# Optimization experiments

Hardware: AMD Instinct MI355X
Metric: run time of the kernel (lower is better)

The kernel has to match this reference:

```python
import math
import jax, jax.numpy as jnp
import numpy as np

NH, NKV, HD, THETA = 32, 8, 128, 500000.0

def rotate_half(x):
    x1, x2 = jnp.split(x, 2, axis=-1)
    return jnp.concatenate((-x2, x1), axis=-1)

def rope_cos_sin(seq_len, dim, base, dtype):
    inv_freq = 1.0 / (base ** (jnp.arange(0, dim, 2, dtype=jnp.float32) / dim))
    t = jnp.arange(seq_len, dtype=jnp.float32)
    freqs = jnp.outer(t, inv_freq)              # [S, dim/2]
    emb = jnp.concatenate((freqs, freqs), -1)   # [S, dim]
    return jnp.cos(emb).astype(dtype), jnp.sin(emb).astype(dtype)

def setup_inputs() -> dict:
    key = jax.random.key(0)
    ks = jax.random.split(key, 5)
    B, S, H = 1, 2048, 4096
    sc = 1.0 / math.sqrt(H)
    return {
        'x':  jax.random.normal(ks[0], (B, S, H), jnp.float32),
        'wq': jax.random.normal(ks[1], (H, H), jnp.float32) * sc,
        'wk': jax.random.normal(ks[2], (NKV * HD, H), jnp.float32) * sc,
        'wv': jax.random.normal(ks[3], (NKV * HD, H), jnp.float32) * sc,
        'wo': jax.random.normal(ks[4], (H, H), jnp.float32) * sc,
    }

def attention(x, wq, wk, wv, wo):
    B, S, H = x.shape
    n_rep = NH // NKV
    q = (x @ wq.T).reshape(B, S, NH, HD).transpose(0, 2, 1, 3)    # [B,NH,S,HD]
    k = (x @ wk.T).reshape(B, S, NKV, HD).transpose(0, 2, 1, 3)   # [B,NKV,S,HD]
    v = (x @ wv.T).reshape(B, S, NKV, HD).transpose(0, 2, 1, 3)
    cos, sin = rope_cos_sin(S, HD, THETA, x.dtype)                # [S,HD]
    cos = cos[None, None]; sin = sin[None, None]
    q = q * cos + rotate_half(q) * sin
    k = k * cos + rotate_half(k) * sin
    k = jnp.repeat(k, n_rep, axis=1)                               # [B,NH,S,HD]
    v = jnp.repeat(v, n_rep, axis=1)
    scores = jnp.einsum('bhqd,bhkd->bhqk', q, k) / math.sqrt(HD)
    causal = jnp.tril(jnp.ones((S, S), dtype=bool))
    scores = jnp.where(causal, scores, jnp.finfo(scores.dtype).min)
    probs = jax.nn.softmax(scores, axis=-1)
    out = jnp.einsum('bhqk,bhkd->bhqd', probs, v)                  # [B,NH,S,HD]
    out = out.transpose(0, 2, 1, 3).reshape(B, S, H)
    return out @ wo.T

def reference(x, wq, wk, wv, wo):
    return attention(x, wq, wk, wv, wo)
```

## Files before the change

kernel.cpp:

```cpp
#include <hip/hip_runtime.h>
#include <hip/hip_bf16.h>
#include <math.h>

typedef __bf16 bf16x8 __attribute__((ext_vector_type(8)));
typedef __bf16 bf16x4 __attribute__((ext_vector_type(4)));
typedef unsigned short u16x8 __attribute__((ext_vector_type(8)));
typedef float  f32x4  __attribute__((ext_vector_type(4)));

constexpr int kS   = 2048;
constexpr int kH   = 4096;
constexpr int kNH  = 32;
constexpr int kNKV = 8;
constexpr int kHD  = 128;
constexpr int kQKV = kH + 2 * kNKV * kHD;
constexpr int kKOff = kH;
constexpr int kVOff = kH + kNKV * kHD;

__global__ void cast_bf16(const float* __restrict__ in, __bf16* __restrict__ out, int n4) {
    int i = blockIdx.x * blockDim.x + threadIdx.x;
    if (i < n4) {
        float4 f = ((const float4*)in)[i];
        bf16x4 o;
        o[0] = (__bf16)f.x; o[1] = (__bf16)f.y; o[2] = (__bf16)f.z; o[3] = (__bf16)f.w;
        ((bf16x4*)out)[i] = o;
    }
}

__global__ void cast_all(const float* __restrict__ x, const float* __restrict__ wq,
                         const float* __restrict__ wk, const float* __restrict__ wv,
                         __bf16* __restrict__ xb, __bf16* __restrict__ wqkv) {
    int i = blockIdx.x * 256 + threadIdx.x;
    float4 f;
    __bf16* dst;
    int di;
    if (i < (1 << 21)) {
        f = ((const float4*)x)[i];
        dst = xb; di = i;
    } else {
        int j = i - (1 << 21);
        const float4* s = (j < (1 << 22)) ? ((const float4*)wq + j)
                        : (j < (5 << 20)) ? ((const float4*)wk + (j - (1 << 22)))
                                          : ((const float4*)wv + (j - (5 << 20)));
        f = *s;
        dst = wqkv; di = j;
    }
    bf16x4 o;
    o[0] = (__bf16)f.x; o[1] = (__bf16)f.y; o[2] = (__bf16)f.z; o[3] = (__bf16)f.w;
    ((bf16x4*)dst)[di] = o;
}

__device__ inline void gld16(const __bf16* g, __bf16* l) {
    __builtin_amdgcn_global_load_lds((const __attribute__((address_space(1))) void*)g,
                                     (__attribute__((address_space(3))) void*)l, 16, 0, 0);
}

constexpr int GBK = 32, GBM = 128;

template <typename OutT, int GBN>
__global__ __launch_bounds__(512, 2) void gemm8(const __bf16* __restrict__ A,
                                                const __bf16* __restrict__ B,
                                                OutT* __restrict__ C,
                                                int M, int N, int K, int nbx) {
    constexpr int FM  = 4;
    constexpr int FN  = GBN / 64;
    constexpr int AL  = GBM / 128;
    constexpr int BL  = GBN / 128;
    constexpr int GPK = AL + BL;
    constexpr int ASZ = GBM * GBK;
    constexpr int BSZ = GBN * GBK;

    __shared__ __align__(16) __bf16 Ab[4][ASZ];
    __shared__ __align__(16) __bf16 Bb[4][BSZ];

    const int tid = threadIdx.x, w = tid >> 6, lane = tid & 63;
    const int lr = lane & 15, g = lane >> 4;

    const int nwg = (int)gridDim.x;
    const int bid = (int)blockIdx.x;
    const int id2 = (bid & 7) * (nwg >> 3) + (bid >> 3);
    const int m0 = (id2 / nbx) * GBM, n0 = (id2 % nbx) * GBN;

    const int wm = (w >> 2) * 64, wn = (w & 3) * (GBN / 4);

    const __bf16* ga[AL]; int la[AL];
    const __bf16* gb[BL]; int lb[BL];
#pragma unroll
    for (int a = 0; a < AL; a++) {
        int G = a * 512 + tid, row = G >> 2;
        int lg = (G & 3) ^ ((row >> 1) & 3);
        ga[a] = A + (size_t)(m0 + row) * K + lg * 8;
        la[a] = G * 8;
    }
#pragma unroll
    for (int b = 0; b < BL; b++) {
        int G = b * 512 + tid, row = G >> 2;
        int lg = (G & 3) ^ ((row >> 1) & 3);
        gb[b] = B + (size_t)(n0 + row) * K + lg * 8;
        lb[b] = G * 8;
    }

    int pao[FM], pbo[FN];
    const int sw = (lr >> 1) & 3;
#pragma unroll
    for (int i = 0; i < FM; i++) pao[i] = (wm + i * 16 + lr) * GBK + ((g ^ sw) * 8);
#pragma unroll
    for (int j = 0; j < FN; j++) pbo[j] = (wn + j * 16 + lr) * GBK + ((g ^ sw) * 8);

    f32x4 acc[FM][FN];
#pragma unroll
    for (int i = 0; i < FM; i++)
#pragma unroll
        for (int j = 0; j < FN; j++) acc[i][j] = (f32x4)(0.f);

    const int NT = K / GBK;

#pragma unroll
    for (int z = 0; z < 3; z++) {
#pragma unroll
        for (int a = 0; a < AL; a++) gld16(ga[a] + z * GBK, &Ab[z][la[a]]);
#pragma unroll
        for (int b = 0; b < BL; b++) gld16(gb[b] + z * GBK, &Bb[z][lb[b]]);
    }
    if constexpr (GPK == 4) asm volatile("s_waitcnt vmcnt(8)" ::: "memory");
    else                    asm volatile("s_waitcnt vmcnt(6)" ::: "memory");
    __builtin_amdgcn_s_barrier();

    for (int Z = 0; Z < NT; ++Z) {
        const int q = Z & 3, qs = (Z + 3) & 3;

        bf16x8 af[FM], bfr[FN];
#pragma unroll
        for (int i = 0; i < FM; i++) af[i]  = *(const bf16x8*)&Ab[q][pao[i]];
#pragma unroll
        for (int j = 0; j < FN; j++) bfr[j] = *(const bf16x8*)&Bb[q][pbo[j]];

        if (Z < NT - 3) {
#pragma unroll
            for (int a = 0; a < AL; a++) gld16(ga[a] + (Z + 3) * GBK, &Ab[qs][la[a]]);
#pragma unroll
            for (int b = 0; b < BL; b++) gld16(gb[b] + (Z + 3) * GBK, &Bb[qs][lb[b]]);
        }

        __builtin_amdgcn_s_barrier();
        __builtin_amdgcn_s_setprio(1);
#pragma unroll
        for (int i = 0; i < FM; i++)
#pragma unroll
            for (int j = 0; j < FN; j++)
                acc[i][j] = __builtin_amdgcn_mfma_f32_16x16x32_bf16(
                    af[i], bfr[j], acc[i][j], 0, 0, 0);
        __builtin_amdgcn_s_setprio(0);

        if (Z < NT - 3) {
            if constexpr (GPK == 4) asm volatile("s_waitcnt vmcnt(8)" ::: "memory");
            else                    asm volatile("s_waitcnt vmcnt(6)" ::: "memory");
        } else if (Z == NT - 3) {
            if constexpr (GPK == 4) asm volatile("s_waitcnt vmcnt(4)" ::: "memory");
            else                    asm volatile("s_waitcnt vmcnt(3)" ::: "memory");
        } else if (Z == NT - 2) {
            asm volatile("s_waitcnt vmcnt(0)" ::: "memory");
        }
        __builtin_amdgcn_s_barrier();
    }

    const int cr = g * 4, cc = lr;
#pragma unroll
    for (int i = 0; i < FM; i++)
#pragma unroll
        for (int j = 0; j < FN; j++) {
            OutT* Cp = C + (size_t)(m0 + wm + i * 16 + cr) * N + (n0 + wn + j * 16 + cc);
#pragma unroll
            for (int r = 0; r < 4; r++) Cp[(size_t)r * N] = (OutT)acc[i][j][r];
        }
}

__global__ void rope_qkv(__bf16* __restrict__ qkv) {
    int idx  = blockIdx.x * 256 + threadIdx.x;
    int d8   = idx & 7;
    int rest = idx >> 3;
    int hh   = rest % (kNH + kNKV);
    int s    = rest / (kNH + kNKV);
    __bf16* base = qkv + (size_t)s * kQKV + ((hh < kNH) ? hh * kHD : kKOff + (hh - kNH) * kHD);
    float sc = (hh < kNH) ? 0.088388347648318447f : 1.0f;
    bf16x8 va = *(const bf16x8*)(base + d8 * 8);
    bf16x8 vb = *(const bf16x8*)(base + 64 + d8 * 8);
    bf16x8 ra, rb;
#pragma unroll
    for (int j = 0; j < 8; j++) {
        int d = d8 * 8 + j;
        float rev = (float)s * exp2f(fmaf((float)d, -0.2958057589f, -2.6514961295f));
        rev -= floorf(rev);
        float ang = rev * 6.28318530718f;
        float sn = __sinf(ang), cs = __cosf(ang);
        float a = (float)va[j], b = (float)vb[j];
        ra[j] = (__bf16)((a * cs - b * sn) * sc);
        rb[j] = (__bf16)((b * cs + a * sn) * sc);
    }
    *(bf16x8*)(base + d8 * 8)      = ra;
    *(bf16x8*)(base + 64 + d8 * 8) = rb;
}

constexpr int VTP = 72;

__global__ __launch_bounds__(256) void flash_attn(const __bf16* __restrict__ qkv,
                                                  __bf16* __restrict__ ob) {
    __shared__ __align__(16) __bf16 Ks[64 * 128];
    __shared__ __align__(16) __bf16 Vt[128 * VTP];
    __shared__ __align__(16) __bf16 Ps[4 * 16 * 64];

    const int tid  = threadIdx.x;
    const int wave = tid >> 6, lane = tid & 63;
    const int bx   = blockIdx.x;
    const int kvh  = bx & 7;
    const int qt   = 127 - (bx >> 3);
    const int h    = kvh * 4 + wave;
    const int r    = lane & 15, g = lane >> 4;
    const int r7   = r & 7;
    const int qglob = qt * 16 + r;

    __bf16* Pw = Ps + wave * 16 * 64;
    const __bf16* kbase = qkv + kKOff + kvh * kHD;
    const __bf16* vbase = qkv + kVOff + kvh * kHD;

    int krow[4], kgc[4];
#pragma unroll
    for (int c = 0; c < 4; c++) {
        krow[c] = wave * 16 + c * 4 + (lane >> 4);
        kgc[c]  = (lane & 15) ^ (krow[c] & 15);
    }

    bf16x8 qfrag[4];
    const __bf16* qrow = qkv + (size_t)(qt * 16 + r) * kQKV + h * kHD + g * 8;
#pragma unroll
    for (int c = 0; c < 4; c++) qfrag[c] = *(const bf16x8*)(qrow + c * 32);

    f32x4 o[8];
#pragma unroll
    for (int dt = 0; dt < 8; dt++) o[dt] = (f32x4)(0.f);
    float mrow = -3.0e38f, lrow = 0.f;

    const int nkt = qt / 4 + 1;
    for (int kt = 0; kt < nkt; ++kt) {
#pragma unroll
        for (int c = 0; c < 4; c++)
            gld16(kbase + (size_t)(kt * 64 + krow[c]) * kQKV + kgc[c] * 8,
                  Ks + (wave * 4 + c) * 512);
#pragma unroll
        for (int i = 0; i < 2; i++) {
            int task = i * 256 + tid;
            int p = task & 31, c = task >> 5;
            const __bf16* v0 = vbase + (size_t)(kt * 64 + 2 * p) * kQKV + c * 8;
            u16x8 a = __builtin_bit_cast(u16x8, *(const bf16x8*)v0);
            u16x8 b = __builtin_bit_cast(u16x8, *(const bf16x8*)(v0 + kQKV));
#pragma unroll
            for (int j = 0; j < 8; j++) {
                unsigned int pk = (unsigned int)a[j] | ((unsigned int)b[j] << 16);
                *(unsigned int*)(Vt + (c * 8 + j) * VTP + 2 * p) = pk;
            }
        }
        __syncthreads();

        f32x4 st[4];
#pragma unroll
        for (int t = 0; t < 4; t++) st[t] = (f32x4)(0.f);
#pragma unroll
        for (int c = 0; c < 4; c++) {
#pragma unroll
            for (int t = 0; t < 4; t++) {
                bf16x8 kf = *(const bf16x8*)&Ks[(t * 16 + r) * 128 + (((c * 4 + g) ^ r) * 8)];
                st[t] = __builtin_amdgcn_mfma_f32_16x16x32_bf16(kf, qfrag[c], st[t], 0, 0, 0);
            }
        }

        if (kt == nkt - 1) {
#pragma unroll
            for (int t = 0; t < 4; t++)
#pragma unroll
                for (int reg = 0; reg < 4; reg++) {
                    int key = kt * 64 + t * 16 + g * 4 + reg;
                    if (key > qglob) st[t][reg] = -3.0e38f;
                }
        }

        float mloc = -3.0e38f;
#pragma unroll
        for (int t = 0; t < 4; t++)
#pragma unroll
            for (int reg = 0; reg < 4; reg++) mloc = fmaxf(mloc, st[t][reg]);
        mloc = fmaxf(mloc, __shfl_xor(mloc, 16));
        mloc = fmaxf(mloc, __shfl_xor(mloc, 32));
        float mnew  = fmaxf(mrow, mloc);
        float alpha = __expf(mrow - mnew);
        mrow = mnew;
        float lsum = 0.f;
#pragma unroll
        for (int t = 0; t < 4; t++)
#pragma unroll
            for (int reg = 0; reg < 4; reg++) {
                float pv = __expf(st[t][reg] - mnew);
                st[t][reg] = pv;
                lsum += pv;
            }
        lsum += __shfl_xor(lsum, 16);
        lsum += __shfl_xor(lsum, 32);
        lrow = lrow * alpha + lsum;

        float ar[4];
#pragma unroll
        for (int reg = 0; reg < 4; reg++) ar[reg] = __shfl(alpha, g * 4 + reg);
#pragma unroll
        for (int dt = 0; dt < 8; dt++)
#pragma unroll
            for (int reg = 0; reg < 4; reg++) o[dt][reg] *= ar[reg];

#pragma unroll
        for (int t = 0; t < 4; t++) {
            bf16x4 pb;
#pragma unroll
            for (int j = 0; j < 4; j++) pb[j] = (__bf16)st[t][j];
            int p8 = t * 4 + g;
            *(bf16x4*)&Pw[r * 64 + (((p8 >> 1) ^ r7) * 8) + ((p8 & 1) * 4)] = pb;
        }
        __asm__ volatile("s_waitcnt lgkmcnt(0)" ::: "memory");

#pragma unroll
        for (int kc = 0; kc < 2; kc++) {
            bf16x8 pf = *(const bf16x8*)&Pw[r * 64 + (((kc * 4 + g) ^ r7) * 8)];
#pragma unroll
            for (int dt = 0; dt < 8; dt++) {
                bf16x8 vf = *(const bf16x8*)&Vt[(dt * 16 + r) * VTP + kc * 32 + g * 8];
                o[dt] = __builtin_amdgcn_mfma_f32_16x16x32_bf16(pf, vf, o[dt], 0, 0, 0);
            }
        }
        __syncthreads();
    }

    float linv = 1.f / lrow;
    float lr4[4];
#pragma unroll
    for (int reg = 0; reg < 4; reg++) lr4[reg] = __shfl(linv, g * 4 + reg);
#pragma unroll
    for (int dt = 0; dt < 8; dt++)
#pragma unroll
        for (int reg = 0; reg < 4; reg++) {
            int qq = g * 4 + reg, dd = dt * 16 + r;
            ob[(size_t)(qt * 16 + qq) * kH + h * kHD + dd] = (__bf16)(o[dt][reg] * lr4[reg]);
        }
}

extern "C" void kernel_launch(void* const* d_in, const int* in_sizes, int n_in,
                              void* d_out, int out_size, void* d_ws, size_t ws_size,
                              hipStream_t stream) {
    const float* x  = (const float*)d_in[0];
    const float* wq = (const float*)d_in[1];
    const float* wk = (const float*)d_in[2];
    const float* wv = (const float*)d_in[3];
    const float* wo = (const float*)d_in[4];
    float* out = (float*)d_out;

    char* p = (char*)d_ws;
    auto alloc = [&](size_t bytes) {
        char* r = p;
        p += (bytes + 255) & ~(size_t)255;
        return r;
    };
    __bf16* xb    = (__bf16*)alloc((size_t)kS * kH * 2);
    __bf16* wqkvb = (__bf16*)alloc((size_t)kQKV * kH * 2);
    __bf16* qkv   = (__bf16*)alloc((size_t)kS * kQKV * 2);
    __bf16* ao    = xb;
    __bf16* wob   = wqkvb;

    cast_all<<<dim3(1 << 15), 256, 0, stream>>>(x, wq, wk, wv, xb, wqkvb);

    gemm8<__bf16, 384><<<dim3((kS / GBM) * (kQKV / 384)), 512, 0, stream>>>(
        xb, wqkvb, qkv, kS, kQKV, kH, kQKV / 384);

    rope_qkv<<<dim3(kS * (kNH + kNKV) * 8 / 256), 256, 0, stream>>>(qkv);

    cast_bf16<<<dim3((kH * kH / 4) / 256), 256, 0, stream>>>(wo, wob, kH * kH / 4);

    flash_attn<<<dim3(kNKV * (kS / 16)), 256, 0, stream>>>(qkv, ao);

    gemm8<float, 256><<<dim3((kS / GBM) * (kH / 256)), 512, 0, stream>>>(
        ao, wob, out, kS, kH, kH, kH / 256);
}
```

Before: 474.9 us.

## Split GEMM k-step into two half phases and remap tiles per XCD

Each k-iteration of the bf16 GEMM is split into two halves: first load A fragments and half the B fragments, issue A prefetches, run half the MFMAs, then load the rest of B and issue B prefetches before the second half of the MFMAs. This interleaves LDS reads and global-to-LDS loads with matrix math more finely, in the style of ping-pong scheduling. It also adds a special tile mapping for the 256-block, 16-column-tile case so that each XCD covers a compact 4x8 block of output tiles, which is meant to improve L2 reuse. The cost is an extra barrier per iteration.

```diff
diff --git a/kernel.cpp b/kernel.cpp
--- a/kernel.cpp
+++ b/kernel.cpp
@@ -63,6 +63,7 @@
                                                 int M, int N, int K, int nbx) {
     constexpr int FM  = 4;
     constexpr int FN  = GBN / 64;
+    constexpr int SH  = FN / 2;
     constexpr int AL  = GBM / 128;
     constexpr int BL  = GBN / 128;
     constexpr int GPK = AL + BL;
@@ -77,8 +78,16 @@
 
     const int nwg = (int)gridDim.x;
     const int bid = (int)blockIdx.x;
-    const int id2 = (bid & 7) * (nwg >> 3) + (bid >> 3);
-    const int m0 = (id2 / nbx) * GBM, n0 = (id2 % nbx) * GBN;
+    int trow, tcol;
+    if (nwg == 256 && nbx == 16) {
+        const int xcd = bid & 7, j = bid >> 3;
+        trow = (xcd >> 1) * 4 + (j >> 3);
+        tcol = (xcd & 1) * 8 + (j & 7);
+    } else {
+        const int id2 = (bid & 7) * (nwg >> 3) + (bid >> 3);
+        trow = id2 / nbx; tcol = id2 % nbx;
+    }
+    const int m0 = trow * GBM, n0 = tcol * GBN;
 
     const int wm = (w >> 2) * 64, wn = (w & 3) * (GBN / 4);
 
@@ -127,26 +136,40 @@
 
     for (int Z = 0; Z < NT; ++Z) {
         const int q = Z & 3, qs = (Z + 3) & 3;
+        const bool stg = Z < NT - 3;
 
         bf16x8 af[FM], bfr[FN];
 #pragma unroll
-        for (int i = 0; i < FM; i++) af[i]  = *(const bf16x8*)&Ab[q][pao[i]];
-#pragma unroll
-        for (int j = 0; j < FN; j++) bfr[j] = *(const bf16x8*)&Bb[q][pbo[j]];
-
-        if (Z < NT - 3) {
+        for (int i = 0; i < FM; i++) af[i] = *(const bf16x8*)&Ab[q][pao[i]];
+#pragma unroll
+        for (int j = 0; j < SH; j++) bfr[j] = *(const bf16x8*)&Bb[q][pbo[j]];
+        if (stg) {
 #pragma unroll
             for (int a = 0; a < AL; a++) gld16(ga[a] + (Z + 3) * GBK, &Ab[qs][la[a]]);
-#pragma unroll
-            for (int b = 0; b < BL; b++) gld16(gb[b] + (Z + 3) * GBK, &Bb[qs][lb[b]]);
-        }
-
+        }
         __builtin_amdgcn_s_barrier();
         __builtin_amdgcn_s_setprio(1);
 #pragma unroll
         for (int i = 0; i < FM; i++)
 #pragma unroll
-            for (int j = 0; j < FN; j++)
+            for (int j = 0; j < SH; j++)
+                acc[i][j] = __builtin_amdgcn_mfma_f32_16x16x32_bf16(
+                    af[i], bfr[j], acc[i][j], 0, 0, 0);
+        __builtin_amdgcn_s_setprio(0);
+        __builtin_amdgcn_s_barrier();
+
+#pragma unroll
+        for (int j = SH; j < FN; j++) bfr[j] = *(const bf16x8*)&Bb[q][pbo[j]];
+        if (stg) {
+#pragma unroll
+            for (int b = 0; b < BL; b++) gld16(gb[b] + (Z + 3) * GBK, &Bb[qs][lb[b]]);
+        }
+        __builtin_amdgcn_s_barrier();
+        __builtin_amdgcn_s_setprio(1);
+#pragma unroll
+        for (int i = 0; i < FM; i++)
+#pragma unroll
+            for (int j = SH; j < FN; j++)
                 acc[i][j] = __builtin_amdgcn_mfma_f32_16x16x32_bf16(
                     af[i], bfr[j], acc[i][j], 0, 0, 0);
         __builtin_amdgcn_s_setprio(0);
```

After: 488.7 us. +2.9%, slower.

## Double-buffer K/V tiles in flash attention and remap GEMM tiles per XCD

Applied to the files above, without the earlier changes.

The flash-attention kernel now keeps two shared-memory buffers for K and transposed V. It issues global loads for the next key tile before the current tile's QK and softmax work, then writes the transposed V into the alternate buffer, so memory latency overlaps compute. Separately, the GEMM tile mapping for the 256-workgroup, 16-column case assigns each XCD a compact 4x8 block of tiles to improve L2 locality. The cost is double the K/V shared memory, which may lower occupancy, plus extra registers held for the prefetched V.

```diff
diff --git a/kernel.cpp b/kernel.cpp
--- a/kernel.cpp
+++ b/kernel.cpp
@@ -77,8 +77,16 @@
 
     const int nwg = (int)gridDim.x;
     const int bid = (int)blockIdx.x;
-    const int id2 = (bid & 7) * (nwg >> 3) + (bid >> 3);
-    const int m0 = (id2 / nbx) * GBM, n0 = (id2 % nbx) * GBN;
+    int trow, tcol;
+    if (nwg == 256 && nbx == 16) {
+        const int xcd = bid & 7, j = bid >> 3;
+        trow = (xcd >> 1) * 4 + (j >> 3);
+        tcol = (xcd & 1) * 8 + (j & 7);
+    } else {
+        const int id2 = (bid & 7) * (nwg >> 3) + (bid >> 3);
+        trow = id2 / nbx; tcol = id2 % nbx;
+    }
+    const int m0 = trow * GBM, n0 = tcol * GBN;
 
     const int wm = (w >> 2) * 64, wn = (w & 3) * (GBN / 4);
 
@@ -204,8 +212,8 @@
 
 __global__ __launch_bounds__(256) void flash_attn(const __bf16* __restrict__ qkv,
                                                   __bf16* __restrict__ ob) {
-    __shared__ __align__(16) __bf16 Ks[64 * 128];
-    __shared__ __align__(16) __bf16 Vt[128 * VTP];
+    __shared__ __align__(16) __bf16 Ks[2][64 * 128];
+    __shared__ __align__(16) __bf16 Vt[2][128 * VTP];
     __shared__ __align__(16) __bf16 Ps[4 * 16 * 64];
 
     const int tid  = threadIdx.x;
@@ -228,6 +236,12 @@
         krow[c] = wave * 16 + c * 4 + (lane >> 4);
         kgc[c]  = (lane & 15) ^ (krow[c] & 15);
     }
+    int vp[2], vc[2];
+#pragma unroll
+    for (int i = 0; i < 2; i++) {
+        int task = i * 256 + tid;
+        vp[i] = task & 31; vc[i] = task >> 5;
+    }
 
     bf16x8 qfrag[4];
     const __bf16* qrow = qkv + (size_t)(qt * 16 + r) * kQKV + h * kHD + g * 8;
@@ -240,25 +254,46 @@
     float mrow = -3.0e38f, lrow = 0.f;
 
     const int nkt = qt / 4 + 1;
+
+    bf16x8 va[2], vb[2];
+#pragma unroll
+    for (int c = 0; c < 4; c++)
+        gld16(kbase + (size_t)krow[c] * kQKV + kgc[c] * 8, &Ks[0][(wave * 4 + c) * 512]);
+#pragma unroll
+    for (int i = 0; i < 2; i++) {
+        const __bf16* v0 = vbase + (size_t)(2 * vp[i]) * kQKV + vc[i] * 8;
+        va[i] = *(const bf16x8*)v0;
+        vb[i] = *(const bf16x8*)(v0 + kQKV);
+    }
+    asm volatile("s_waitcnt vmcnt(0)" ::: "memory");
+#pragma unroll
+    for (int i = 0; i < 2; i++) {
+        u16x8 a = __builtin_bit_cast(u16x8, va[i]);
+        u16x8 b = __builtin_bit_cast(u16x8, vb[i]);
+#pragma unroll
+        for (int j = 0; j < 8; j++) {
+            unsigned int pk = (unsigned int)a[j] | ((unsigned int)b[j] << 16);
+            *(unsigned int*)(&Vt[0][(vc[i] * 8 + j) * VTP + 2 * vp[i]]) = pk;
+        }
+    }
+    __syncthreads();
+
     for (int kt = 0; kt < nkt; ++kt) {
-#pragma unroll
-        for (int c = 0; c < 4; c++)
-            gld16(kbase + (size_t)(kt * 64 + krow[c]) * kQKV + kgc[c] * 8,
-                  Ks + (wave * 4 + c) * 512);
-#pragma unroll
-        for (int i = 0; i < 2; i++) {
-            int task = i * 256 + tid;
-            int p = task & 31, c = task >> 5;
-            const __bf16* v0 = vbase + (size_t)(kt * 64 + 2 * p) * kQKV + c * 8;
-            u16x8 a = __builtin_bit_cast(u16x8, *(const bf16x8*)v0);
-            u16x8 b = __builtin_bit_cast(u16x8, *(const bf16x8*)(v0 + kQKV));
-#pragma unroll
-            for (int j = 0; j < 8; j++) {
-                unsigned int pk = (unsigned int)a[j] | ((unsigned int)b[j] << 16);
-                *(unsigned int*)(Vt + (c * 8 + j) * VTP + 2 * p) = pk;
+        const int cur = kt & 1, nb = cur ^ 1;
+        const bool nxt = (kt + 1) < nkt;
+
+        if (nxt) {
+#pragma unroll
+            for (int c = 0; c < 4; c++)
+                gld16(kbase + (size_t)((kt + 1) * 64 + krow[c]) * kQKV + kgc[c] * 8,
+                      &Ks[nb][(wave * 4 + c) * 512]);
+#pragma unroll
+            for (int i = 0; i < 2; i++) {
+                const __bf16* v0 = vbase + (size_t)((kt + 1) * 64 + 2 * vp[i]) * kQKV + vc[i] * 8;
+                va[i] = *(const bf16x8*)v0;
+                vb[i] = *(const bf16x8*)(v0 + kQKV);
             }
         }
-        __syncthreads();
 
         f32x4 st[4];
 #pragma unroll
@@ -267,7 +302,7 @@
         for (int c = 0; c < 4; c++) {
 #pragma unroll
             for (int t = 0; t < 4; t++) {
-                bf16x8 kf = *(const bf16x8*)&Ks[(t * 16 + r) * 128 + (((c * 4 + g) ^ r) * 8)];
+                bf16x8 kf = *(const bf16x8*)&Ks[cur][(t * 16 + r) * 128 + (((c * 4 + g) ^ r) * 8)];
                 st[t] = __builtin_amdgcn_mfma_f32_16x16x32_bf16(kf, qfrag[c], st[t], 0, 0, 0);
             }
         }
@@ -313,6 +348,20 @@
 #pragma unroll
             for (int reg = 0; reg < 4; reg++) o[dt][reg] *= ar[reg];
 
+        if (nxt) {
+            asm volatile("s_waitcnt vmcnt(0)" ::: "memory");
+#pragma unroll
+            for (int i = 0; i < 2; i++) {
+                u16x8 a = __builtin_bit_cast(u16x8, va[i]);
+                u16x8 b = __builtin_bit_cast(u16x8, vb[i]);
+#pragma unroll
+                for (int j = 0; j < 8; j++) {
+                    unsigned int pk = (unsigned int)a[j] | ((unsigned int)b[j] << 16);
+                    *(unsigned int*)(&Vt[nb][(vc[i] * 8 + j) * VTP + 2 * vp[i]]) = pk;
+                }
+            }
+        }
+
 #pragma unroll
         for (int t = 0; t < 4; t++) {
             bf16x4 pb;
@@ -328,7 +377,7 @@
             bf16x8 pf = *(const bf16x8*)&Pw[r * 64 + (((kc * 4 + g) ^ r7) * 8)];
 #pragma unroll
             for (int dt = 0; dt < 8; dt++) {
-                bf16x8 vf = *(const bf16x8*)&Vt[(dt * 16 + r) * VTP + kc * 32 + g * 8];
+                bf16x8 vf = *(const bf16x8*)&Vt[cur][(dt * 16 + r) * VTP + kc * 32 + g * 8];
                 o[dt] = __builtin_amdgcn_mfma_f32_16x16x32_bf16(pf, vf, o[dt], 0, 0, 0);
             }
         }
```

New measurement: 472.1 us. No clear change (-0.6%).
